# Performance work log

Measured on AMD Instinct MI355X. Metric: run time of the kernel, lower is better.

Reference implementation:

```python
import jax, jax.numpy as jnp
import numpy as np
from jax import lax

DIM = 192
HEADS = 4
EPS = 1e-12  # torch F.normalize eps


def setup_inputs() -> dict:
    key = jax.random.key(0)
    k1, k2, k3, k4 = jax.random.split(key, 4)
    b, c, h, w = 8, DIM, 128, 128
    x = jax.random.normal(k1, (b, c, h, w), dtype=jnp.float32)
    w_qkv = jax.random.normal(k2, (3 * c, c), dtype=jnp.float32) * (1.0 / np.sqrt(c))
    w_dw = jax.random.normal(k3, (3 * c, 1, 3, 3), dtype=jnp.float32) * (1.0 / 3.0)
    temperature = jnp.ones((HEADS, 1, 1), dtype=jnp.float32)
    w_proj = jax.random.normal(k4, (c, c), dtype=jnp.float32) * (1.0 / np.sqrt(c))
    return {"x": x, "w_qkv": w_qkv, "w_dw": w_dw, "temperature": temperature, "w_proj": w_proj}


def _l2norm(t):
    # torch F.normalize(dim=-1): t / max(||t||_2, eps)
    n = jnp.sqrt(jnp.sum(t * t, axis=-1, keepdims=True))
    return t / jnp.maximum(n, EPS)


def reference(x, w_qkv, w_dw, temperature, w_proj):
    b, c, h, w = x.shape
    heads = HEADS
    hc = c // heads  # channels per head
    # 1x1 conv: dim -> 3*dim
    qkv = jnp.einsum('bchw,oc->bohw', x, w_qkv)
    # depthwise 3x3 conv, padding=1, no relu/norm
    qkv = lax.conv_general_dilated(
        qkv, w_dw, window_strides=(1, 1), padding='SAME',
        feature_group_count=3 * c,
        dimension_numbers=('NCHW', 'OIHW', 'NCHW'))
    q, k, v = jnp.split(qkv, 3, axis=1)
    # b (head c) h w -> b head c (h w)
    n = h * w
    q = q.reshape(b, heads, hc, n)
    k = k.reshape(b, heads, hc, n)
    v = v.reshape(b, heads, hc, n)
    q = _l2norm(q)
    k = _l2norm(k)
    # channel attention: [b, head, hc, hc]
    attn = jnp.einsum('bhcn,bhdn->bhcd', q, k) * temperature[None]
    attn = jax.nn.softmax(attn, axis=-1)
    out = jnp.einsum('bhcd,bhdn->bhcn', attn, v)
    out = out.reshape(b, c, h, w)
    out = jnp.einsum('bchw,oc->bohw', out, w_proj)
    return out
```

## Files before the change

kernel.cpp:

```cpp
#include <hip/hip_runtime.h>
#include <stdint.h>


typedef __attribute__((ext_vector_type(8))) short bf16x8;
typedef __attribute__((ext_vector_type(4))) float f32x4;
typedef __attribute__((ext_vector_type(2))) float f32x2;
typedef __attribute__((ext_vector_type(4))) unsigned int u32x4;
typedef __attribute__((ext_vector_type(2))) unsigned int u32x2;
typedef unsigned short u16;

#define HW 16384
#define CD 192
#define O3 576
#define KD 192

__device__ __forceinline__ float b2f(u16 u) {
    union { unsigned int i; float f; } v; v.i = ((unsigned int)u) << 16; return v.f;
}
__device__ __forceinline__ u16 f2b(float f) {
    union { float f; unsigned int i; } v; v.f = f;
    return (u16)((v.i + 0x7fffu + ((v.i >> 16) & 1u)) >> 16);
}

__global__ __launch_bounds__(256) void fill_f32(float* p, long long n, float val) {
    long long stride = (long long)gridDim.x * 256;
    for (long long i = blockIdx.x * 256LL + threadIdx.x; i < n; i += stride) p[i] = val;
}

__global__ __launch_bounds__(256) void zerof(float* p, int n) {
    int i = blockIdx.x * 256 + threadIdx.x;
    if (i < n) p[i] = 0.f;
}

__global__ __launch_bounds__(256) void afrag_prep(
    const float* __restrict__ W, u16* __restrict__ Af, int M, int NF)
{
    int t = blockIdx.x * 256 + threadIdx.x;
    if (t >= NF * 64) return;
    int F = t >> 6, lane = t & 63;
    int ks = F % 6, mt = (F / 6) & 3, rwmb = F / 24;
    int row = rwmb * 64 + mt * 16 + (lane & 15);
    int k0 = ks * 32 + (lane >> 4) * 8;
    u16 v[8] __attribute__((aligned(16)));
    if (row < M) {
        const float* src = W + (long long)row * KD + k0;
#pragma unroll
        for (int j = 0; j < 8; j++) v[j] = f2b(src[j]);
    } else {
#pragma unroll
        for (int j = 0; j < 8; j++) v[j] = 0;
    }
    *(bf16x8*)&Af[(long long)F * 512 + lane * 8] = *(const bf16x8*)v;
}

template <bool SRC_F32, bool OUT_F32, int NMS>
__global__ __launch_bounds__(256, 2) void gemm_tn(
    const u16* __restrict__ Afrag, const void* __restrict__ Bsrc, void* __restrict__ Cv,
    long long af_bs, long long b_bs, long long c_bs)
{
    __shared__ u16 lsB[128 * 192];
    const int tid = threadIdx.x, lane = tid & 63, wid = tid >> 6;
    const int n0 = blockIdx.x * 128;
    const long long bz = blockIdx.z;
    const int lr = lane & 15, quad = lane >> 4;
    const int wn = wid & 1, wm = wid >> 1;

#define LADDR(n_, ks_) ((n_) * 192 + (((ks_) ^ (((n_) >> 2) & 7)) * 8))

    if (SRC_F32) {
        const int c32 = lane & 31, rs = lane >> 5;
        const float* gp = (const float*)Bsrc + bz * b_bs + n0 + 4 * c32;
        f32x4 bufA[8], bufB[8];
#define LOADC_F(buf, c) do { \
    const float* p_ = gp + (long long)((c) * 64 + wid * 16 + rs * 8) * HW; \
    _Pragma("unroll") for (int i_ = 0; i_ < 8; i_++) \
        buf[i_] = *(const f32x4*)(p_ + (long long)i_ * HW); \
} while (0)
#define PROC_F(buf, c) do { \
    const int kslot_ = (c) * 8 + wid * 2 + rs; \
    _Pragma("unroll") for (int j_ = 0; j_ < 4; j_++) { \
        const int n_ = 4 * c32 + j_; \
        unsigned int p0_, p1_, p2_, p3_; \
        asm("v_cvt_pk_bf16_f32 %0, %1, %2" : "=v"(p0_) : "v"(buf[0][j_]), "v"(buf[1][j_])); \
        asm("v_cvt_pk_bf16_f32 %0, %1, %2" : "=v"(p1_) : "v"(buf[2][j_]), "v"(buf[3][j_])); \
        asm("v_cvt_pk_bf16_f32 %0, %1, %2" : "=v"(p2_) : "v"(buf[4][j_]), "v"(buf[5][j_])); \
        asm("v_cvt_pk_bf16_f32 %0, %1, %2" : "=v"(p3_) : "v"(buf[6][j_]), "v"(buf[7][j_])); \
        *(u32x4*)&lsB[LADDR(n_, kslot_)] = (u32x4){p0_, p1_, p2_, p3_}; \
    } \
} while (0)
        LOADC_F(bufA, 0);
        LOADC_F(bufB, 1);
        __builtin_amdgcn_sched_barrier(0);
        PROC_F(bufA, 0);
        LOADC_F(bufA, 2);
        __builtin_amdgcn_sched_barrier(0);
        PROC_F(bufB, 1);
        PROC_F(bufA, 2);
#undef LOADC_F
#undef PROC_F
    } else {
        const int c16 = lane & 15, rs4 = lane >> 4;
        const u16* gp = (const u16*)Bsrc + bz * b_bs + n0 + 8 * c16;
        u32x4 bufA[4], bufB[4];
#define LOADC_B(buf, c) do { \
    const u16* p_ = gp + (long long)((c) * 64 + wid * 16 + rs4 * 4) * HW; \
    _Pragma("unroll") for (int i_ = 0; i_ < 4; i_++) \
        buf[i_] = *(const u32x4*)(p_ + (long long)i_ * HW); \
} while (0)
#define PROC_B(buf, c) do { \
    const int kslot_ = (c) * 8 + wid * 2 + (rs4 >> 1); \
    const int kh_ = (rs4 & 1) * 4; \
    _Pragma("unroll") for (int j_ = 0; j_ < 4; j_++) { \
        unsigned int l0_ = __builtin_amdgcn_perm(buf[0][j_], buf[1][j_], 0x01000504u); \
        unsigned int l1_ = __builtin_amdgcn_perm(buf[2][j_], buf[3][j_], 0x01000504u); \
        unsigned int h0_ = __builtin_amdgcn_perm(buf[0][j_], buf[1][j_], 0x03020706u); \
        unsigned int h1_ = __builtin_amdgcn_perm(buf[2][j_], buf[3][j_], 0x03020706u); \
        *(u32x2*)&lsB[LADDR(8 * c16 + 2 * j_, kslot_) + kh_] = (u32x2){l0_, l1_}; \
        *(u32x2*)&lsB[LADDR(8 * c16 + 2 * j_ + 1, kslot_) + kh_] = (u32x2){h0_, h1_}; \
    } \
} while (0)
        LOADC_B(bufA, 0);
        LOADC_B(bufB, 1);
        __builtin_amdgcn_sched_barrier(0);
        PROC_B(bufA, 0);
        LOADC_B(bufA, 2);
        __builtin_amdgcn_sched_barrier(0);
        PROC_B(bufB, 1);
        PROC_B(bufA, 2);
#undef LOADC_B
#undef PROC_B
    }
    __syncthreads();

    bf16x8 bfv[6][4];
#pragma unroll
    for (int ks = 0; ks < 6; ks++)
#pragma unroll
        for (int nt = 0; nt < 4; nt++) {
            const int n_ = wn * 64 + nt * 16 + lr;
            bfv[ks][nt] = *(const bf16x8*)&lsB[LADDR(n_, ks * 4 + quad)];
        }
#undef LADDR

    const u16* ApBase = Afrag + bz * af_bs + lane * 8;
    const long long cB = bz * c_bs + n0 + wn * 64 + lr;
    constexpr int NT = NMS / 2;

#define LOAD_AF(dst, sv) do { \
    _Pragma("unroll") for (int mtl_ = 0; mtl_ < 2; mtl_++) \
    _Pragma("unroll") for (int ks_ = 0; ks_ < 6; ks_++) \
        dst[mtl_][ks_] = *(const bf16x8*)(ApBase + \
            (long long)(((sv) >> 1) * 24 + (((sv) & 1) * 2 + mtl_) * 6 + ks_) * 512); \
} while (0)
#define COMPUTE_MB(afb, sv) do { \
    f32x4 acc_[2][4]; \
    _Pragma("unroll") for (int i_ = 0; i_ < 2; i_++) \
    _Pragma("unroll") for (int j_ = 0; j_ < 4; j_++) \
        acc_[i_][j_] = (f32x4){0.f, 0.f, 0.f, 0.f}; \
    _Pragma("unroll") for (int ks_ = 0; ks_ < 6; ks_++) \
    _Pragma("unroll") for (int mtl_ = 0; mtl_ < 2; mtl_++) \
    _Pragma("unroll") for (int nt_ = 0; nt_ < 4; nt_++) \
        acc_[mtl_][nt_] = __builtin_amdgcn_mfma_f32_16x16x32_bf16( \
            afb[mtl_][ks_], bfv[ks_][nt_], acc_[mtl_][nt_], 0, 0, 0); \
    _Pragma("unroll") for (int mtl_ = 0; mtl_ < 2; mtl_++) \
    _Pragma("unroll") for (int r_ = 0; r_ < 4; r_++) { \
        const long long ro_ = cB + (long long)(32 * (sv) + mtl_ * 16 + quad * 4 + r_) * HW; \
        _Pragma("unroll") for (int nt_ = 0; nt_ < 4; nt_++) { \
            if (OUT_F32) ((float*)Cv)[ro_ + nt_ * 16] = acc_[mtl_][nt_][r_]; \
            else         ((u16*)Cv)[ro_ + nt_ * 16] = f2b(acc_[mtl_][nt_][r_]); \
        } \
    } \
} while (0)

    bf16x8 afA[2][6], afB[2][6];
    const int s0 = wm * NT;
    LOAD_AF(afA, s0);
#pragma unroll
    for (int t = 0; t < NT; ++t) {
        if (t + 1 < NT) {
            if (t & 1) LOAD_AF(afA, s0 + t + 1);
            else       LOAD_AF(afB, s0 + t + 1);
            __builtin_amdgcn_sched_barrier(0);
        }
        if (t & 1) COMPUTE_MB(afB, s0 + t);
        else       COMPUTE_MB(afA, s0 + t);
    }
#undef LOAD_AF
#undef COMPUTE_MB
}

__global__ __launch_bounds__(256) void dwconv2(
    const u16* __restrict__ in, const float* __restrict__ wdw, u16* __restrict__ outp,
    long long in_bs, long long out_bs, int wch0)
{
    const int rt = blockIdx.x, ch = blockIdx.y, tid = threadIdx.x;
    const long long bz = blockIdx.z;
    const u16* ip = in + bz * in_bs + (long long)ch * HW;
    u16* op = outp + bz * out_bs + (long long)ch * HW;
    __shared__ float t[18 * 132];
    const int r0 = rt * 16;
    if (tid < 18) {
        t[tid * 132 + 0] = 0.f;   t[tid * 132 + 129] = 0.f;
        t[tid * 132 + 130] = 0.f; t[tid * 132 + 131] = 0.f;
    }
    for (int i = tid; i < 288; i += 256) {
        int rr = i >> 4, cc = (i & 15) * 8;
        int gr = r0 + rr - 1;
        float f[8];
        if (gr >= 0 && gr < 128) {
            bf16x8 v = *(const bf16x8*)(ip + gr * 128 + cc);
#pragma unroll
            for (int j = 0; j < 8; j++) f[j] = b2f((u16)v[j]);
        } else {
#pragma unroll
            for (int j = 0; j < 8; j++) f[j] = 0.f;
        }
#pragma unroll
        for (int j = 0; j < 8; j++) t[rr * 132 + 1 + cc + j] = f[j];
    }
    float w[9];
#pragma unroll
    for (int j = 0; j < 9; j++) w[j] = wdw[(wch0 + ch) * 9 + j];
    __syncthreads();
    const int rr = tid >> 4, c8 = (tid & 15) * 8;
    float o[8] = {0.f, 0.f, 0.f, 0.f, 0.f, 0.f, 0.f, 0.f};
#pragma unroll
    for (int dy = 0; dy < 3; dy++) {
        const float* row = &t[(rr + dy) * 132 + c8];
        float r[12] __attribute__((aligned(16)));
        *(f32x4*)&r[0] = *(const f32x4*)row;
        *(f32x4*)&r[4] = *(const f32x4*)(row + 4);
        *(f32x4*)&r[8] = *(const f32x4*)(row + 8);
        const float w0 = w[dy * 3], w1 = w[dy * 3 + 1], w2 = w[dy * 3 + 2];
#pragma unroll
        for (int j = 0; j < 8; j++) o[j] += w0 * r[j] + w1 * r[j + 1] + w2 * r[j + 2];
    }
    u16 ob[8] __attribute__((aligned(16)));
#pragma unroll
    for (int j = 0; j < 8; j++) ob[j] = f2b(o[j]);
    *(bf16x8*)&op[(long long)(r0 + rr) * 128 + c8] = *(const bf16x8*)ob;
}

__global__ __launch_bounds__(256) void attn_scores(
    const u16* __restrict__ qk, float* __restrict__ S, float* __restrict__ norms,
    int bh0)
{
    const int tid = threadIdx.x, lane = tid & 63, wid = tid >> 6;
    const int kc = blockIdx.x, head = blockIdx.y;
    const long long bz = blockIdx.z;
    const u16* q = qk + bz * (2LL * CD * HW) + (long long)head * 48 * HW;
    const u16* k = q + (long long)CD * HW;
    const int lr = lane & 15, quad = lane >> 4;

    f32x4 sc[3][3], sq[3], sk[3];
#pragma unroll
    for (int i = 0; i < 3; i++) {
#pragma unroll
        for (int j = 0; j < 3; j++) sc[i][j] = (f32x4){0.f, 0.f, 0.f, 0.f};
        sq[i] = (f32x4){0.f, 0.f, 0.f, 0.f};
        sk[i] = (f32x4){0.f, 0.f, 0.f, 0.f};
    }
    const int n0 = kc * 1024 + wid * 256;
#pragma unroll 2
    for (int s = 0; s < 8; s++) {
        const int n = n0 + s * 32 + quad * 8;
        bf16x8 aq[3], ak[3];
#pragma unroll
        for (int t3 = 0; t3 < 3; t3++) {
            aq[t3] = *(const bf16x8*)(q + (long long)(t3 * 16 + lr) * HW + n);
            ak[t3] = *(const bf16x8*)(k + (long long)(t3 * 16 + lr) * HW + n);
        }
#pragma unroll
        for (int mt = 0; mt < 3; mt++)
#pragma unroll
            for (int nt = 0; nt < 3; nt++)
                sc[mt][nt] = __builtin_amdgcn_mfma_f32_16x16x32_bf16(aq[mt], ak[nt], sc[mt][nt], 0, 0, 0);
#pragma unroll
        for (int t3 = 0; t3 < 3; t3++) {
            sq[t3] = __builtin_amdgcn_mfma_f32_16x16x32_bf16(aq[t3], aq[t3], sq[t3], 0, 0, 0);
            sk[t3] = __builtin_amdgcn_mfma_f32_16x16x32_bf16(ak[t3], ak[t3], sk[t3], 0, 0, 0);
        }
    }
    __shared__ float sS[2304];
    __shared__ float snq[48], snk[48];
    for (int i = tid; i < 2304; i += 256) sS[i] = 0.f;
    if (tid < 48) { snq[tid] = 0.f; snk[tid] = 0.f; }
    __syncthreads();
#pragma unroll
    for (int mt = 0; mt < 3; mt++)
#pragma unroll
        for (int nt = 0; nt < 3; nt++)
#pragma unroll
            for (int r = 0; r < 4; r++)
                atomicAdd(&sS[(mt * 16 + quad * 4 + r) * 48 + nt * 16 + lr], sc[mt][nt][r]);
#pragma unroll
    for (int t3 = 0; t3 < 3; t3++)
#pragma unroll
        for (int r = 0; r < 4; r++) {
            int rw = quad * 4 + r;
            if (rw == lr) {
                atomicAdd(&snq[t3 * 16 + rw], sq[t3][r]);
                atomicAdd(&snk[t3 * 16 + rw], sk[t3][r]);
            }
        }
    __syncthreads();
    const int bh = bh0 + (int)bz * 4 + head;
    float* Sg = S + (long long)bh * 2304;
    for (int i = tid; i < 2304; i += 256) atomicAdd(&Sg[i], sS[i]);
    float* ng = norms + bh * 96;
    if (tid < 48) atomicAdd(&ng[tid], snq[tid]);
    else if (tid < 96) atomicAdd(&ng[tid], snk[tid - 48]);
}

__global__ __launch_bounds__(256) void mproj_sm(
    const float* __restrict__ wproj, const float* __restrict__ S,
    const float* __restrict__ norms, const float* __restrict__ temp,
    u16* __restrict__ Mm, int b0)
{
    const int ob = blockIdx.x, b = b0 + blockIdx.y, tid = threadIdx.x;
    __shared__ float sA[9216];
    if (tid < 192) {
        const int h = tid / 48, r = tid - h * 48;
        const int bh = b * 4 + h;
        const float tv = temp[h];
        const float* Sg = S + (long long)bh * 2304;
        const float* ng = norms + bh * 96;
        const float nq = fmaxf(sqrtf(ng[r]), 1e-12f);
        float lg[48];
        float mx = -1e30f;
#pragma unroll
        for (int d = 0; d < 48; d++) {
            float nk = fmaxf(sqrtf(ng[48 + d]), 1e-12f);
            float v = Sg[r * 48 + d] * tv / (nq * nk);
            lg[d] = v; mx = fmaxf(mx, v);
        }
        float sum = 0.f;
#pragma unroll
        for (int d = 0; d < 48; d++) { float e = __expf(lg[d] - mx); lg[d] = e; sum += e; }
        const float inv = 1.f / sum;
#pragma unroll
        for (int d = 0; d < 48; d++) sA[h * 2304 + r * 48 + d] = lg[d] * inv;
    }
    __syncthreads();
    for (int i = tid; i < 48 * 192; i += 256) {
        int o = ob * 48 + i / 192;
        int cc = i % 192;
        int h = cc / 48, d = cc - h * 48;
        const float* wr = wproj + o * 192 + h * 48;
        const float* ar = &sA[h * 2304 + d];
        float acc = 0.f;
        for (int c = 0; c < 48; c++) acc += wr[c] * ar[c * 48];
        int fi = (o >> 6) * 24 + ((o >> 4) & 3) * 6 + (cc >> 5);
        int lanei = ((cc >> 3) & 3) * 16 + (o & 15);
        Mm[(long long)b * 49152 + (long long)fi * 512 + lanei * 8 + (cc & 7)] = f2b(acc);
    }
}

extern "C" void kernel_launch(void* const* d_in, const int* in_sizes, int n_in,
                              void* d_out, int out_size, void* d_ws, size_t ws_size,
                              hipStream_t stream)
{
    const float* x     = (const float*)d_in[0];
    const float* wqkv  = (const float*)d_in[1];
    const float* wdw   = (const float*)d_in[2];
    const float* temp  = (const float*)d_in[3];
    const float* wproj = (const float*)d_in[4];
    float* out = (float*)d_out;
    char* ws = (char*)d_ws;
    const long long CHW = (long long)CD * HW;

    if (ws_size < 2097152ULL + 31457280ULL) {
        fill_f32<<<2048, 256, 0, stream>>>(out, out_size, 100.0f);
        return;
    }
    int G = 8;
    while (G > 1 && (unsigned long long)(2097152ULL + (unsigned long long)G * 31457280ULL) > (unsigned long long)ws_size)
        G >>= 1;

    float* S      = (float*)ws;
    float* norms  = (float*)(ws + 294912);
    u16*   MmF    = (u16*)(ws + 602112);
    u16*   wqkvF  = (u16*)(ws + 1388544);
    u16* region1  = (u16*)(ws + 2097152);
    u16* qkv_pre  = region1 + (long long)G * 2 * CHW;

    zerof<<<300, 256, 0, stream>>>(S, 76800);
    afrag_prep<<<60, 256, 0, stream>>>(wqkv, wqkvF, O3, 240);

    for (int g0 = 0; g0 < 8; g0 += G) {
        gemm_tn<true, false, 18><<<dim3(128, 1, G), 256, 0, stream>>>(
            wqkvF, x + (long long)g0 * CHW, qkv_pre, 0LL, CHW, 3LL * CHW);
        dwconv2<<<dim3(8, 384, G), 256, 0, stream>>>(
            qkv_pre, wdw, region1, 3LL * CHW, 2LL * CHW, 0);
        dwconv2<<<dim3(8, 192, G), 256, 0, stream>>>(
            qkv_pre + 2LL * CHW, wdw, qkv_pre, 3LL * CHW, 3LL * CHW, 384);
        attn_scores<<<dim3(16, 4, G), 256, 0, stream>>>(region1, S, norms, g0 * 4);
        mproj_sm<<<dim3(4, G), 256, 0, stream>>>(wproj, S, norms, temp, MmF, g0);
        gemm_tn<false, true, 6><<<dim3(128, 1, G), 256, 0, stream>>>(
            MmF + (long long)g0 * 49152, qkv_pre, out + (long long)g0 * CHW,
            49152LL, 3LL * CHW, CHW);
    }
}
```

Before: 386.3 us.

## Fuse q/k depthwise conv into attention-score kernel

The separate depthwise 3x3 conv pass over the q and k channels is removed. The attention-score kernel now reads the pre-conv qkv buffer and computes each 8-pixel q/k fragment on the fly, using per-lane weights held in registers and packed bf16 conversion. This avoids writing an intermediate q/k tensor to global memory and reading it back. In exchange, the score kernel does more ALU work and issues halo loads (neighbour rows and edge pixels) on a grid that has few waves, so it may become latency-bound.

Measured after the change: 497.8 us. +28.8%, slower.

```diff
diff --git a/kernel.cpp b/kernel.cpp
--- a/kernel.cpp
+++ b/kernel.cpp
@@ -241,16 +241,55 @@
     *(bf16x8*)&op[(long long)(r0 + rr) * 128 + c8] = *(const bf16x8*)ob;
 }
 
-__global__ __launch_bounds__(256) void attn_scores(
-    const u16* __restrict__ qk, float* __restrict__ S, float* __restrict__ norms,
-    int bh0)
+__device__ __forceinline__ bf16x8 dw8(const u16* __restrict__ ip,
+                                      const float (&w9)[9], int r, int c0)
+{
+    float o[8] = {0.f, 0.f, 0.f, 0.f, 0.f, 0.f, 0.f, 0.f};
+#pragma unroll
+    for (int dy = 0; dy < 3; dy++) {
+        const int rr = r - 1 + dy;
+        if (rr >= 0 && rr < 128) {
+            const u16* rp = ip + rr * 128 + c0;
+            float f[10];
+            f[0] = (c0 > 0) ? b2f(rp[-1]) : 0.f;
+            bf16x8 v = *(const bf16x8*)rp;
+#pragma unroll
+            for (int j = 0; j < 8; j++) f[j + 1] = b2f((u16)v[j]);
+            f[9] = (c0 < 120) ? b2f(rp[8]) : 0.f;
+            const float w0 = w9[dy * 3], w1 = w9[dy * 3 + 1], w2 = w9[dy * 3 + 2];
+#pragma unroll
+            for (int j = 0; j < 8; j++) o[j] += w0 * f[j] + w1 * f[j + 1] + w2 * f[j + 2];
+        }
+    }
+    union { u32x4 u; bf16x8 b; } pk;
+    asm("v_cvt_pk_bf16_f32 %0, %1, %2" : "=v"(pk.u[0]) : "v"(o[0]), "v"(o[1]));
+    asm("v_cvt_pk_bf16_f32 %0, %1, %2" : "=v"(pk.u[1]) : "v"(o[2]), "v"(o[3]));
+    asm("v_cvt_pk_bf16_f32 %0, %1, %2" : "=v"(pk.u[2]) : "v"(o[4]), "v"(o[5]));
+    asm("v_cvt_pk_bf16_f32 %0, %1, %2" : "=v"(pk.u[3]) : "v"(o[6]), "v"(o[7]));
+    return pk.b;
+}
+
+__global__ __launch_bounds__(256) void attn_fused(
+    const u16* __restrict__ qkv, const float* __restrict__ wdw,
+    float* __restrict__ S, float* __restrict__ norms, int bh0)
 {
     const int tid = threadIdx.x, lane = tid & 63, wid = tid >> 6;
     const int kc = blockIdx.x, head = blockIdx.y;
     const long long bz = blockIdx.z;
-    const u16* q = qk + bz * (2LL * CD * HW) + (long long)head * 48 * HW;
-    const u16* k = q + (long long)CD * HW;
+    const u16* qb = qkv + bz * (3LL * CD * HW) + (long long)(head * 48) * HW;
+    const u16* kb = qb + (long long)CD * HW;
     const int lr = lane & 15, quad = lane >> 4;
+
+    float wq[3][9], wk[3][9];
+#pragma unroll
+    for (int t3 = 0; t3 < 3; t3++) {
+        const int ch = head * 48 + t3 * 16 + lr;
+#pragma unroll
+        for (int j = 0; j < 9; j++) {
+            wq[t3][j] = wdw[ch * 9 + j];
+            wk[t3][j] = wdw[(CD + ch) * 9 + j];
+        }
+    }
 
     f32x4 sc[3][3], sq[3], sk[3];
 #pragma unroll
@@ -261,14 +300,16 @@
         sk[i] = (f32x4){0.f, 0.f, 0.f, 0.f};
     }
     const int n0 = kc * 1024 + wid * 256;
-#pragma unroll 2
     for (int s = 0; s < 8; s++) {
-        const int n = n0 + s * 32 + quad * 8;
+        const int nabs = n0 + s * 32 + quad * 8;
+        const int r = nabs >> 7;
+        const int c0 = nabs & 127;
         bf16x8 aq[3], ak[3];
 #pragma unroll
         for (int t3 = 0; t3 < 3; t3++) {
-            aq[t3] = *(const bf16x8*)(q + (long long)(t3 * 16 + lr) * HW + n);
-            ak[t3] = *(const bf16x8*)(k + (long long)(t3 * 16 + lr) * HW + n);
+            const long long co = (long long)(t3 * 16 + lr) * HW;
+            aq[t3] = dw8(qb + co, wq[t3], r, c0);
+            ak[t3] = dw8(kb + co, wk[t3], r, c0);
         }
 #pragma unroll
         for (int mt = 0; mt < 3; mt++)
@@ -390,11 +431,10 @@
     for (int g0 = 0; g0 < 8; g0 += G) {
         gemm_tn<true, false, 18><<<dim3(128, 1, G), 256, 0, stream>>>(
             wqkvF, x + (long long)g0 * CHW, qkv_pre, 0LL, CHW, 3LL * CHW);
-        dwconv2<<<dim3(8, 384, G), 256, 0, stream>>>(
-            qkv_pre, wdw, region1, 3LL * CHW, 2LL * CHW, 0);
+        attn_fused<<<dim3(16, 4, G), 256, 0, stream>>>(
+            qkv_pre, wdw, S, norms, g0 * 4);
         dwconv2<<<dim3(8, 192, G), 256, 0, stream>>>(
             qkv_pre + 2LL * CHW, wdw, qkv_pre, 3LL * CHW, 3LL * CHW, 384);
-        attn_scores<<<dim3(16, 4, G), 256, 0, stream>>>(region1, S, norms, g0 * 4);
         mproj_sm<<<dim3(4, G), 256, 0, stream>>>(wproj, S, norms, temp, MmF, g0);
         gemm_tn<false, true, 6><<<dim3(128, 1, G), 256, 0, stream>>>(
             MmF + (long long)g0 * 49152, qkv_pre, out + (long long)g0 * CHW,
```
